# Kernel tuning notes

Hardware: AMD Instinct MI355X
Metric: run time of the kernel (lower is better)

## Reference

```python
import jax, jax.numpy as jnp
import numpy as np


def setup_inputs() -> dict:
    key = jax.random.key(0)
    ks = jax.random.split(key, 8)
    B, S, K, D = 2, 64, 64, 256
    C = D // 8
    return {
        "x": jax.random.normal(ks[0], (B, S, K, D), dtype=jnp.float32),
        "Wq": jax.random.normal(ks[1], (C, D), dtype=jnp.float32) * (1.0 / np.sqrt(D)),
        "bq": jax.random.normal(ks[2], (C,), dtype=jnp.float32) * 0.01,
        "Wk": jax.random.normal(ks[3], (C, D), dtype=jnp.float32) * (1.0 / np.sqrt(D)),
        "bk": jax.random.normal(ks[4], (C,), dtype=jnp.float32) * 0.01,
        "Wv": jax.random.normal(ks[5], (D, D), dtype=jnp.float32) * (1.0 / np.sqrt(D)),
        "bv": jax.random.normal(ks[6], (D,), dtype=jnp.float32) * 0.01,
        "gamma": jax.random.uniform(ks[7], (1,), dtype=jnp.float32),
    }


def reference(x, Wq, bq, Wk, bk, Wv, bv, gamma):
    # x: [B, S, K, D]
    B, S, K, D = x.shape
    N = K * S
    # torch: x.permute(0,3,2,1) -> [B, D, K, S]; flatten (K,S) -> N (n = k*S + s)
    xp = jnp.transpose(x, (0, 3, 2, 1)).reshape(B, D, N)  # [B, D, N]
    # 1x1 convs == per-token linear maps over the channel dim
    q = jnp.einsum('cd,bdn->bnc', Wq, xp) + bq            # [B, N, C]
    k = jnp.einsum('cd,bdn->bcn', Wk, xp) + bk[:, None]   # [B, C, N]
    energy = jnp.einsum('bnc,bcm->bnm', q, k)             # [B, N, N]
    attention = jax.nn.softmax(energy, axis=-1)           # rows sum to 1
    v = jnp.einsum('ed,bdn->ben', Wv, xp) + bv[:, None]   # [B, D, N]
    # out[b,d,i] = sum_j V[b,d,j] * A[b,i,j]
    out = jnp.einsum('bdj,bij->bdi', v, attention)        # [B, D, N]
    out = gamma * out + xp                                # residual with learned scale
    out = out.reshape(B, D, K, S)
    return jnp.transpose(out, (0, 3, 2, 1))               # [B, S, K, D]
```

## Files before the change

kernel.cpp:

```cpp
#include <hip/hip_runtime.h>
#include <stdint.h>
#include <math.h>

using short8   = __attribute__((ext_vector_type(8))) short;
using ushort4v = __attribute__((ext_vector_type(4))) unsigned short;
using f32x4    = __attribute__((ext_vector_type(4))) float;
using uint4v   = __attribute__((ext_vector_type(4))) unsigned int;
using uint2v   = __attribute__((ext_vector_type(2))) unsigned int;

#define B_ 2
#define S_ 64
#define K_ 64
#define D_ 256
#define C_ 32
#define N_ 4096
#define LOG2E 1.4426950408889634f

__device__ __forceinline__ float b2f(unsigned short u) {
    unsigned int v = ((unsigned int)u) << 16;
    return __builtin_bit_cast(float, v);
}
__device__ __forceinline__ unsigned short f2b(float f) {
    unsigned int x = __builtin_bit_cast(unsigned int, f);
    x += 0x7fffu + ((x >> 16) & 1u);
    return (unsigned short)(x >> 16);
}
__device__ __forceinline__ unsigned int pk2(float a, float b) {
    unsigned int xa = __builtin_bit_cast(unsigned int, a);
    unsigned int xb = __builtin_bit_cast(unsigned int, b);
    xa += 0x7fffu + ((xa >> 16) & 1u);
    xb += 0x7fffu + ((xb >> 16) & 1u);
    return (xa >> 16) | (xb & 0xffff0000u);
}

__global__ __launch_bounds__(256) void wcvt_kernel(
    const float* __restrict__ Wq, const float* __restrict__ bq,
    const float* __restrict__ Wk, const float* __restrict__ bk,
    const float* __restrict__ Wv, const float* __restrict__ bv,
    unsigned short* __restrict__ Wh, unsigned short* __restrict__ Wl,
    float* __restrict__ bcat)
{
    int oc = blockIdx.x;
    int d  = threadIdx.x;
    float w;
    if (oc < 32)       w = Wq[oc * 256 + d] * LOG2E;
    else if (oc < 64)  w = Wk[(oc - 32) * 256 + d];
    else               w = Wv[(oc - 64) * 256 + d];
    unsigned short h = f2b(w);
    Wh[oc * 256 + d] = h;
    Wl[oc * 256 + d] = f2b(w - b2f(h));
    if (d == 0) {
        float bb;
        if (oc < 32)      bb = bq[oc] * LOG2E;
        else if (oc < 64) bb = bk[oc - 32];
        else              bb = bv[oc - 64];
        bcat[oc] = bb;
    }
}

__global__ __launch_bounds__(512) void qkv_kernel(
    const float* __restrict__ x,
    const unsigned short* __restrict__ Wh, const unsigned short* __restrict__ Wl,
    const float* __restrict__ bcat,
    unsigned short* __restrict__ Qh, unsigned short* __restrict__ Ql,
    unsigned short* __restrict__ Kh, unsigned short* __restrict__ Kl,
    unsigned short* __restrict__ Vm)
{
    __shared__ unsigned short lxh[16 * 256];
    __shared__ unsigned short lxl[16 * 256];

    int tid = threadIdx.x;
    int bid = blockIdx.x;
    int b  = bid >> 8;
    int n0 = (bid & 255) << 4;

    {
        int tt = tid >> 5, m = tid & 31;
        int n = n0 + tt;
        int s = n & 63, kk = n >> 6;
        const float* xr = x + (((size_t)(b * S_ + s)) * K_ + kk) * D_ + m * 8;
        short8 h8, l8;
#pragma unroll
        for (int e = 0; e < 8; ++e) {
            float v = xr[e];
            unsigned short hh = f2b(v);
            h8[e] = (short)hh; l8[e] = (short)f2b(v - b2f(hh));
        }
        int sw = ((m ^ (tt & 7)) << 3);
        *(short8*)(lxh + tt * 256 + sw) = h8;
        *(short8*)(lxl + tt * 256 + sw) = l8;
    }
    __syncthreads();

    int wave = tid >> 6, lane = tid & 63;
    int col = lane & 15, g = lane >> 4;

    if (wave < 4) {
        int ct = wave;
        int oc0 = ct * 16;
        const unsigned short* whr = Wh + (size_t)(oc0 + col) * 256;
        const unsigned short* wlr = Wl + (size_t)(oc0 + col) * 256;
        f32x4 acc = {0.f, 0.f, 0.f, 0.f};
#pragma unroll
        for (int dc = 0; dc < 8; ++dc) {
            int sw = (((dc * 4 + g) ^ (col & 7)) << 3);
            short8 xh8 = *(const short8*)(lxh + col * 256 + sw);
            short8 xl8 = *(const short8*)(lxl + col * 256 + sw);
            short8 wh8 = *(const short8*)(whr + dc * 32 + g * 8);
            short8 wl8 = *(const short8*)(wlr + dc * 32 + g * 8);
            acc = __builtin_amdgcn_mfma_f32_16x16x32_bf16(xl8, wh8, acc, 0, 0, 0);
            acc = __builtin_amdgcn_mfma_f32_16x16x32_bf16(xh8, wl8, acc, 0, 0, 0);
            acc = __builtin_amdgcn_mfma_f32_16x16x32_bf16(xh8, wh8, acc, 0, 0, 0);
        }
        float bb = bcat[oc0 + col];
        unsigned short* Th = (ct < 2) ? Qh : Kh;
        unsigned short* Tl = (ct < 2) ? Ql : Kl;
        int c0 = (ct & 1) * 16;
#pragma unroll
        for (int r = 0; r < 4; ++r) {
            int tok = n0 + g * 4 + r;
            float v = acc[r] + bb;
            unsigned short hh = f2b(v);
            size_t idx = ((size_t)b * N_ + tok) * C_ + c0 + col;
            Th[idx] = hh;
            Tl[idx] = f2b(v - b2f(hh));
        }
    } else {
        int i = wave - 4;
#pragma unroll
        for (int k = 0; k < 4; ++k) {
            int ct = 4 + i + 4 * k;
            int oc0 = ct * 16;
            const unsigned short* whr = Wh + (size_t)(oc0 + col) * 256;
            f32x4 acc = {0.f, 0.f, 0.f, 0.f};
#pragma unroll
            for (int dc = 0; dc < 8; ++dc) {
                int sw = (((dc * 4 + g) ^ (col & 7)) << 3);
                short8 xh8 = *(const short8*)(lxh + col * 256 + sw);
                short8 wh8 = *(const short8*)(whr + dc * 32 + g * 8);
                acc = __builtin_amdgcn_mfma_f32_16x16x32_bf16(xh8, wh8, acc, 0, 0, 0);
            }
            float bb = bcat[oc0 + col];
            int c0 = oc0 - 64;
            ushort4v st;
#pragma unroll
            for (int r = 0; r < 4; ++r) st[r] = f2b(acc[r] + bb);
            int tok0 = n0 + g * 4;
            int s0 = 8 * g + ((n0 & 16) >> 2);
            int d_ch = c0 + col;
            int o = d_ch * 64 + s0 * 2;
            o ^= (d_ch & 7) << 4;
            size_t vbyteoff = ((size_t)b * (N_ / 32) + (tok0 >> 5)) * (D_ * 32 * 2)
                            + (size_t)o;
            *(ushort4v*)((char*)Vm + vbyteoff) = st;
        }
    }
}

__global__ __launch_bounds__(1024, 4) void attn_kernel(
    const unsigned short* __restrict__ Qh, const unsigned short* __restrict__ Ql,
    const unsigned short* __restrict__ Kh, const unsigned short* __restrict__ Kl,
    const unsigned short* __restrict__ Vm,
    unsigned short* __restrict__ O_bf16, float* __restrict__ lsum_part)
{
    __shared__ __align__(16) char vlds[2][16384];
    __shared__ __align__(16) char plds[2 * 8192];

    int tid  = threadIdx.x;
    int wave = tid >> 6;
    int lane = tid & 63;
    int col = lane & 15, g = lane >> 4;
    int qq = wave >> 2;
    int dq = wave & 3;
    int kh = dq & 1;
    int qs_own = dq >> 1;
    int tid16 = tid * 16;
    int lane16 = lane * 16;

    int bid = blockIdx.x;
    int x7 = bid & 7;
    int b  = x7 >> 2;
    int ks = x7 & 3;
    int qt = bid >> 3;
    int q0 = qt * 128 + qq * 32;
    int jbase = ks * (N_ / 4);

    size_t qoff = ((size_t)b * N_ + q0 + qs_own * 16 + col) * C_ + g * 8;
    short8 qfh = *(const short8*)(Qh + qoff);
    short8 qfl = *(const short8*)(Ql + qoff);

    f32x4 acc[2][4];
#pragma unroll
    for (int qs = 0; qs < 2; ++qs)
#pragma unroll
        for (int dt = 0; dt < 4; ++dt) acc[qs][dt] = (f32x4){0.f, 0.f, 0.f, 0.f};
    float l_run = 0.f;

    const unsigned short* kbh = Kh + (size_t)b * N_ * C_;
    const unsigned short* kbl = Kl + (size_t)b * N_ * C_;
    const char* vbyte = (const char*)Vm + (size_t)b * ((size_t)N_ * D_ * 2);

    auto kaddr = [&](int it) {
        return (size_t)(jbase + it * 32 + kh * 16 + col) * C_ + g * 8;
    };

    unsigned vro = (unsigned)(((dq * 64 + col) * 64 + g * 16) ^ ((col & 7) << 4));
    int st = qq * 2 + qs_own;
    char* pmy = plds + st * 1024 + lane16 + kh * 8;
    const char* pr0 = plds + (qq * 2) * 1024 + lane16;
    const char* pr1 = plds + (qq * 2 + 1) * 1024 + lane16;

    {
        const char* vsrc = vbyte + (size_t)(ks * 32) * 16384 + tid16;
        *(f32x4*)(vlds[0] + tid16) = *(const f32x4*)(vsrc);
    }
    short8 khA = *(const short8*)(kbh + kaddr(0));
    short8 klA = *(const short8*)(kbl + kaddr(0));
    short8 khB = *(const short8*)(kbh + kaddr(1));
    short8 klB = *(const short8*)(kbl + kaddr(1));
    {
        f32x4 z = {0.f, 0.f, 0.f, 0.f};
        f32x4 sa = __builtin_amdgcn_mfma_f32_16x16x32_bf16(klA, qfh, z, 0, 0, 0);
        sa = __builtin_amdgcn_mfma_f32_16x16x32_bf16(khA, qfl, sa, 0, 0, 0);
        sa = __builtin_amdgcn_mfma_f32_16x16x32_bf16(khA, qfh, sa, 0, 0, 0);
        float pa[4];
#pragma unroll
        for (int r = 0; r < 4; ++r) pa[r] = exp2f(sa[r]);
        l_run += (pa[0] + pa[1]) + (pa[2] + pa[3]);
        uint2v uo;
        uo[0] = pk2(pa[0], pa[1]); uo[1] = pk2(pa[2], pa[3]);
        *(uint2v*)(pmy) = uo;
    }
    __syncthreads();

#define ATTN_PHASE(IT, CKH, CKL, NKH, NKL)                                       \
    {                                                                            \
        int itn_ = (IT) + 1;                                                     \
        int itk_ = (IT) + 2;         \
        const char* vsrc_ = vbyte + (size_t)(ks * 32 + itn_) * 16384 + tid16;    \
        f32x4 stg_ = *(const f32x4*)(vsrc_);                                     \
        NKH = *(const short8*)(kbh + kaddr(itk_));                               \
        NKL = *(const short8*)(kbl + kaddr(itk_));                               \
        __builtin_amdgcn_sched_barrier(0);        \
        f32x4 z_ = {0.f, 0.f, 0.f, 0.f};                                         \
        __builtin_amdgcn_s_setprio(1);                                           \
        f32x4 sa_ = __builtin_amdgcn_mfma_f32_16x16x32_bf16(CKL, qfh, z_, 0, 0, 0); \
        sa_ = __builtin_amdgcn_mfma_f32_16x16x32_bf16(CKH, qfl, sa_, 0, 0, 0);   \
        sa_ = __builtin_amdgcn_mfma_f32_16x16x32_bf16(CKH, qfh, sa_, 0, 0, 0);   \
        __builtin_amdgcn_s_setprio(0);                                           \
        float pa_[4];                                                            \
        _Pragma("unroll")                                                        \
        for (int r = 0; r < 4; ++r) pa_[r] = exp2f(sa_[r]);                      \
        l_run += (pa_[0] + pa_[1]) + (pa_[2] + pa_[3]);                          \
        uint2v uo_;                                                              \
        uo_[0] = pk2(pa_[0], pa_[1]); uo_[1] = pk2(pa_[2], pa_[3]);              \
        int rb_ = (IT) & 1, wb_ = (itn_) & 1;                                    \
        short8 pf0_ = *(const short8*)(pr0 + rb_ * 8192);                        \
        short8 pf1_ = *(const short8*)(pr1 + rb_ * 8192);                        \
        short8 vf_[4];                                                           \
        _Pragma("unroll")                                                        \
        for (int dt = 0; dt < 4; ++dt)                                           \
            vf_[dt] = *(const short8*)(vlds[rb_] + vro + dt * 1024);             \
        __builtin_amdgcn_s_setprio(1);                                           \
        _Pragma("unroll")                                                        \
        for (int dt = 0; dt < 4; ++dt) {                                         \
            acc[0][dt] = __builtin_amdgcn_mfma_f32_16x16x32_bf16(vf_[dt], pf0_, acc[0][dt], 0, 0, 0); \
            acc[1][dt] = __builtin_amdgcn_mfma_f32_16x16x32_bf16(vf_[dt], pf1_, acc[1][dt], 0, 0, 0); \
        }                                                                        \
        __builtin_amdgcn_s_setprio(0);                                           \
        *(uint2v*)(pmy + wb_ * 8192) = uo_;                                      \
        *(f32x4*)(vlds[wb_] + tid16) = stg_;                                     \
        __syncthreads();                                                         \
    }

    for (int it2 = 0; it2 < 15; ++it2) {
        int itA = it2 * 2, itB = itA + 1;
        ATTN_PHASE(itA, khB, klB, khA, klA);
        ATTN_PHASE(itB, khA, klA, khB, klB);
    }
    ATTN_PHASE(30, khB, klB, khA, klA);
#undef ATTN_PHASE

    {
        short8 pf0 = *(const short8*)(pr0 + 8192);
        short8 pf1 = *(const short8*)(pr1 + 8192);
        short8 vf[4];
#pragma unroll
        for (int dt = 0; dt < 4; ++dt)
            vf[dt] = *(const short8*)(vlds[1] + vro + dt * 1024);
#pragma unroll
        for (int dt = 0; dt < 4; ++dt) {
            acc[0][dt] = __builtin_amdgcn_mfma_f32_16x16x32_bf16(vf[dt], pf0, acc[0][dt], 0, 0, 0);
            acc[1][dt] = __builtin_amdgcn_mfma_f32_16x16x32_bf16(vf[dt], pf1, acc[1][dt], 0, 0, 0);
        }
    }

    l_run += __shfl_xor(l_run, 16); l_run += __shfl_xor(l_run, 32);

    unsigned short* op = O_bf16 + (size_t)bid * 32768 + (qq * 2 + (dq >> 1)) * 4096;
#pragma unroll
    for (int qs = 0; qs < 2; ++qs)
#pragma unroll
        for (int dt = 0; dt < 4; ++dt) {
            int j = qs * 8 + (dq & 1) * 4 + dt;
            uint2v uo;
            uo[0] = pk2(acc[qs][dt][0], acc[qs][dt][1]);
            uo[1] = pk2(acc[qs][dt][2], acc[qs][dt][3]);
            *(uint2v*)(op + j * 256 + col * 16 + g * 4) = uo;
        }
    if (g == 0)
        lsum_part[bid * 256 + kh * 128 + qq * 32 + qs_own * 16 + col] = l_run;
}

__global__ __launch_bounds__(256) void epi_kernel(
    const unsigned short* __restrict__ O_bf16, const float* __restrict__ lsum_part,
    const float* __restrict__ x, const float* __restrict__ gamma_p,
    float* __restrict__ out)
{
    int gid = blockIdx.x * 256 + threadIdx.x;
    int d  = (gid & 63) * 4;
    int nl = gid >> 6;
    int b  = nl >> 12;
    int n  = nl & (N_ - 1);

    int qt = n >> 7, qq = (n >> 5) & 3, qs = (n >> 4) & 1, col = n & 15;
    int dh = d >> 7, dt = (d >> 4) & 7;
    int w = qq * 2 + dh, j = qs * 8 + dt;
    int boff = w * 4096 + j * 256 + col * 16 + (d & 15);
    int loff = qq * 32 + qs * 16 + col;

    f32x4 acc = {0.f, 0.f, 0.f, 0.f};
    float l = 0.f;
#pragma unroll
    for (int ks = 0; ks < 4; ++ks) {
        int bid = qt * 8 + b * 4 + ks;
        ushort4v p = *(const ushort4v*)(O_bf16 + (size_t)bid * 32768 + boff);
        acc[0] += b2f(p[0]); acc[1] += b2f(p[1]);
        acc[2] += b2f(p[2]); acc[3] += b2f(p[3]);
        l += lsum_part[bid * 256 + loff] + lsum_part[bid * 256 + 128 + loff];
    }
    float scale = gamma_p[0] / l;
    int s = n & 63, kk = n >> 6;
    size_t o = (((size_t)(b * S_ + s)) * K_ + kk) * D_ + d;
    f32x4 xv = *(const f32x4*)(x + o);
    f32x4 ov;
#pragma unroll
    for (int e = 0; e < 4; ++e) ov[e] = acc[e] * scale + xv[e];
    *(f32x4*)(out + o) = ov;
}

extern "C" void kernel_launch(void* const* d_in, const int* in_sizes, int n_in,
                              void* d_out, int out_size, void* d_ws, size_t ws_size,
                              hipStream_t stream) {
    const float* x  = (const float*)d_in[0];
    const float* Wq = (const float*)d_in[1];
    const float* bq = (const float*)d_in[2];
    const float* Wk = (const float*)d_in[3];
    const float* bk = (const float*)d_in[4];
    const float* Wv = (const float*)d_in[5];
    const float* bv = (const float*)d_in[6];
    const float* gm = (const float*)d_in[7];

    char* ws = (char*)d_ws;
    unsigned short* Wh   = (unsigned short*)(ws);
    unsigned short* Wl   = (unsigned short*)(ws + 0x40000);
    float*          bcat = (float*)         (ws + 0x80000);
    unsigned short* Qh   = (unsigned short*)(ws + 0x100000);
    unsigned short* Ql   = (unsigned short*)(ws + 0x180000);
    unsigned short* Kh   = (unsigned short*)(ws + 0x200000);
    unsigned short* Kl   = (unsigned short*)(ws + 0x280000);
    unsigned short* Vm   = (unsigned short*)(ws + 0x300000);
    unsigned short* Op   = (unsigned short*)(ws + 0x700000);
    float*          lp   = (float*)         (ws + 0x2700000);
    float* o = (float*)d_out;

    wcvt_kernel<<<320, 256, 0, stream>>>(Wq, bq, Wk, bk, Wv, bv, Wh, Wl, bcat);
    qkv_kernel<<<512, 512, 0, stream>>>(x, Wh, Wl, bcat, Qh, Ql, Kh, Kl, Vm);
    attn_kernel<<<256, 1024, 0, stream>>>(Qh, Ql, Kh, Kl, Vm, Op, lp);
    epi_kernel<<<2048, 256, 0, stream>>>(Op, lp, x, gm, o);
}
```

Measured before the change: 62.83 us.

## Halve attention block to 512 threads with each wave owning more work

The attention kernel now runs 8 waves per block instead of 16. Each wave computes scores for both 16-key halves of its query strip and accumulates PV for four query strips instead of two. This removes the duplicated key-half split and cuts barrier participants and redundant V-fragment LDS reads per block. In exchange each wave holds twice the accumulators and does more sequential MFMA work, with fewer waves left to hide latency. The lsum partial layout and the epilogue indexing change to match.

```diff
diff --git a/kernel.cpp b/kernel.cpp
--- a/kernel.cpp
+++ b/kernel.cpp
@@ -157,7 +157,7 @@
     }
 }
 
-__global__ __launch_bounds__(1024, 4) void attn_kernel(
+__global__ __launch_bounds__(512, 2) void attn_kernel(
     const unsigned short* __restrict__ Qh, const unsigned short* __restrict__ Ql,
     const unsigned short* __restrict__ Kh, const unsigned short* __restrict__ Kl,
     const unsigned short* __restrict__ Vm,
@@ -170,11 +170,10 @@
     int wave = tid >> 6;
     int lane = tid & 63;
     int col = lane & 15, g = lane >> 4;
-    int qq = wave >> 2;
-    int dq = wave & 3;
-    int kh = dq & 1;
-    int qs_own = dq >> 1;
-    int tid16 = tid * 16;
+    int qq2 = wave >> 2;
+    int dq  = wave & 3;
+    int st_own = qq2 * 4 + dq;
+    int tid32 = tid * 32;
     int lane16 = lane * 16;
 
     int bid = blockIdx.x;
@@ -182,134 +181,154 @@
     int b  = x7 >> 2;
     int ks = x7 & 3;
     int qt = bid >> 3;
-    int q0 = qt * 128 + qq * 32;
     int jbase = ks * (N_ / 4);
 
-    size_t qoff = ((size_t)b * N_ + q0 + qs_own * 16 + col) * C_ + g * 8;
+    size_t qoff = ((size_t)b * N_ + qt * 128 + st_own * 16 + col) * C_ + g * 8;
     short8 qfh = *(const short8*)(Qh + qoff);
     short8 qfl = *(const short8*)(Ql + qoff);
 
-    f32x4 acc[2][4];
-#pragma unroll
-    for (int qs = 0; qs < 2; ++qs)
-#pragma unroll
-        for (int dt = 0; dt < 4; ++dt) acc[qs][dt] = (f32x4){0.f, 0.f, 0.f, 0.f};
+    f32x4 acc[4][4];
+#pragma unroll
+    for (int s = 0; s < 4; ++s)
+#pragma unroll
+        for (int dt = 0; dt < 4; ++dt) acc[s][dt] = (f32x4){0.f, 0.f, 0.f, 0.f};
     float l_run = 0.f;
 
     const unsigned short* kbh = Kh + (size_t)b * N_ * C_;
     const unsigned short* kbl = Kl + (size_t)b * N_ * C_;
     const char* vbyte = (const char*)Vm + (size_t)b * ((size_t)N_ * D_ * 2);
 
-    auto kaddr = [&](int it) {
-        return (size_t)(jbase + it * 32 + kh * 16 + col) * C_ + g * 8;
+    auto kaddr = [&](int it, int half) {
+        return (size_t)(jbase + it * 32 + half * 16 + col) * C_ + g * 8;
     };
 
     unsigned vro = (unsigned)(((dq * 64 + col) * 64 + g * 16) ^ ((col & 7) << 4));
-    int st = qq * 2 + qs_own;
-    char* pmy = plds + st * 1024 + lane16 + kh * 8;
-    const char* pr0 = plds + (qq * 2) * 1024 + lane16;
-    const char* pr1 = plds + (qq * 2 + 1) * 1024 + lane16;
+    char* pmy = plds + st_own * 1024 + lane16;
+    const char* prg = plds + (qq2 * 4) * 1024 + lane16;
 
     {
-        const char* vsrc = vbyte + (size_t)(ks * 32) * 16384 + tid16;
-        *(f32x4*)(vlds[0] + tid16) = *(const f32x4*)(vsrc);
-    }
-    short8 khA = *(const short8*)(kbh + kaddr(0));
-    short8 klA = *(const short8*)(kbl + kaddr(0));
-    short8 khB = *(const short8*)(kbh + kaddr(1));
-    short8 klB = *(const short8*)(kbl + kaddr(1));
+        const char* vsrc = vbyte + (size_t)(ks * 32) * 16384 + tid32;
+        *(f32x4*)(vlds[0] + tid32)      = *(const f32x4*)(vsrc);
+        *(f32x4*)(vlds[0] + tid32 + 16) = *(const f32x4*)(vsrc + 16);
+    }
+    short8 k0hA = *(const short8*)(kbh + kaddr(0, 0));
+    short8 k0lA = *(const short8*)(kbl + kaddr(0, 0));
+    short8 k1hA = *(const short8*)(kbh + kaddr(0, 1));
+    short8 k1lA = *(const short8*)(kbl + kaddr(0, 1));
+    short8 k0hB = *(const short8*)(kbh + kaddr(1, 0));
+    short8 k0lB = *(const short8*)(kbl + kaddr(1, 0));
+    short8 k1hB = *(const short8*)(kbh + kaddr(1, 1));
+    short8 k1lB = *(const short8*)(kbl + kaddr(1, 1));
     {
         f32x4 z = {0.f, 0.f, 0.f, 0.f};
-        f32x4 sa = __builtin_amdgcn_mfma_f32_16x16x32_bf16(klA, qfh, z, 0, 0, 0);
-        sa = __builtin_amdgcn_mfma_f32_16x16x32_bf16(khA, qfl, sa, 0, 0, 0);
-        sa = __builtin_amdgcn_mfma_f32_16x16x32_bf16(khA, qfh, sa, 0, 0, 0);
-        float pa[4];
-#pragma unroll
-        for (int r = 0; r < 4; ++r) pa[r] = exp2f(sa[r]);
-        l_run += (pa[0] + pa[1]) + (pa[2] + pa[3]);
-        uint2v uo;
-        uo[0] = pk2(pa[0], pa[1]); uo[1] = pk2(pa[2], pa[3]);
-        *(uint2v*)(pmy) = uo;
+        f32x4 s0 = __builtin_amdgcn_mfma_f32_16x16x32_bf16(k0lA, qfh, z, 0, 0, 0);
+        s0 = __builtin_amdgcn_mfma_f32_16x16x32_bf16(k0hA, qfl, s0, 0, 0, 0);
+        s0 = __builtin_amdgcn_mfma_f32_16x16x32_bf16(k0hA, qfh, s0, 0, 0, 0);
+        f32x4 s1 = __builtin_amdgcn_mfma_f32_16x16x32_bf16(k1lA, qfh, z, 0, 0, 0);
+        s1 = __builtin_amdgcn_mfma_f32_16x16x32_bf16(k1hA, qfl, s1, 0, 0, 0);
+        s1 = __builtin_amdgcn_mfma_f32_16x16x32_bf16(k1hA, qfh, s1, 0, 0, 0);
+        float p0[4], p1[4];
+#pragma unroll
+        for (int r = 0; r < 4; ++r) { p0[r] = exp2f(s0[r]); p1[r] = exp2f(s1[r]); }
+        l_run += (p0[0] + p0[1]) + (p0[2] + p0[3]) + (p1[0] + p1[1]) + (p1[2] + p1[3]);
+        uint4v uo;
+        uo[0] = pk2(p0[0], p0[1]); uo[1] = pk2(p0[2], p0[3]);
+        uo[2] = pk2(p1[0], p1[1]); uo[3] = pk2(p1[2], p1[3]);
+        *(uint4v*)(pmy) = uo;
     }
     __syncthreads();
 
-#define ATTN_PHASE(IT, CKH, CKL, NKH, NKL)                                       \
+#define ATTN_PHASE(IT, C0H, C0L, C1H, C1L, N0H, N0L, N1H, N1L)                   \
     {                                                                            \
         int itn_ = (IT) + 1;                                                     \
         int itk_ = (IT) + 2;         \
-        const char* vsrc_ = vbyte + (size_t)(ks * 32 + itn_) * 16384 + tid16;    \
-        f32x4 stg_ = *(const f32x4*)(vsrc_);                                     \
-        NKH = *(const short8*)(kbh + kaddr(itk_));                               \
-        NKL = *(const short8*)(kbl + kaddr(itk_));                               \
+        const char* vsrc_ = vbyte + (size_t)(ks * 32 + itn_) * 16384 + tid32;    \
+        f32x4 stg0_ = *(const f32x4*)(vsrc_);                                    \
+        f32x4 stg1_ = *(const f32x4*)(vsrc_ + 16);                               \
+        N0H = *(const short8*)(kbh + kaddr(itk_, 0));                            \
+        N0L = *(const short8*)(kbl + kaddr(itk_, 0));                            \
+        N1H = *(const short8*)(kbh + kaddr(itk_, 1));                            \
+        N1L = *(const short8*)(kbl + kaddr(itk_, 1));                            \
         __builtin_amdgcn_sched_barrier(0);        \
         f32x4 z_ = {0.f, 0.f, 0.f, 0.f};                                         \
         __builtin_amdgcn_s_setprio(1);                                           \
-        f32x4 sa_ = __builtin_amdgcn_mfma_f32_16x16x32_bf16(CKL, qfh, z_, 0, 0, 0); \
-        sa_ = __builtin_amdgcn_mfma_f32_16x16x32_bf16(CKH, qfl, sa_, 0, 0, 0);   \
-        sa_ = __builtin_amdgcn_mfma_f32_16x16x32_bf16(CKH, qfh, sa_, 0, 0, 0);   \
+        f32x4 s0_ = __builtin_amdgcn_mfma_f32_16x16x32_bf16(C0L, qfh, z_, 0, 0, 0); \
+        s0_ = __builtin_amdgcn_mfma_f32_16x16x32_bf16(C0H, qfl, s0_, 0, 0, 0);   \
+        s0_ = __builtin_amdgcn_mfma_f32_16x16x32_bf16(C0H, qfh, s0_, 0, 0, 0);   \
+        f32x4 s1_ = __builtin_amdgcn_mfma_f32_16x16x32_bf16(C1L, qfh, z_, 0, 0, 0); \
+        s1_ = __builtin_amdgcn_mfma_f32_16x16x32_bf16(C1H, qfl, s1_, 0, 0, 0);   \
+        s1_ = __builtin_amdgcn_mfma_f32_16x16x32_bf16(C1H, qfh, s1_, 0, 0, 0);   \
         __builtin_amdgcn_s_setprio(0);                                           \
-        float pa_[4];                                                            \
+        float p0_[4], p1_[4];                                                    \
         _Pragma("unroll")                                                        \
-        for (int r = 0; r < 4; ++r) pa_[r] = exp2f(sa_[r]);                      \
-        l_run += (pa_[0] + pa_[1]) + (pa_[2] + pa_[3]);                          \
-        uint2v uo_;                                                              \
-        uo_[0] = pk2(pa_[0], pa_[1]); uo_[1] = pk2(pa_[2], pa_[3]);              \
+        for (int r = 0; r < 4; ++r) { p0_[r] = exp2f(s0_[r]); p1_[r] = exp2f(s1_[r]); } \
+        l_run += (p0_[0] + p0_[1]) + (p0_[2] + p0_[3])                           \
+               + (p1_[0] + p1_[1]) + (p1_[2] + p1_[3]);                          \
+        uint4v uo_;                                                              \
+        uo_[0] = pk2(p0_[0], p0_[1]); uo_[1] = pk2(p0_[2], p0_[3]);              \
+        uo_[2] = pk2(p1_[0], p1_[1]); uo_[3] = pk2(p1_[2], p1_[3]);              \
         int rb_ = (IT) & 1, wb_ = (itn_) & 1;                                    \
-        short8 pf0_ = *(const short8*)(pr0 + rb_ * 8192);                        \
-        short8 pf1_ = *(const short8*)(pr1 + rb_ * 8192);                        \
-        short8 vf_[4];                                                           \
+        short8 pf_[4], vf_[4];                                                   \
+        _Pragma("unroll")                                                        \
+        for (int s = 0; s < 4; ++s)                                              \
+            pf_[s] = *(const short8*)(prg + s * 1024 + rb_ * 8192);              \
         _Pragma("unroll")                                                        \
         for (int dt = 0; dt < 4; ++dt)                                           \
             vf_[dt] = *(const short8*)(vlds[rb_] + vro + dt * 1024);             \
         __builtin_amdgcn_s_setprio(1);                                           \
         _Pragma("unroll")                                                        \
-        for (int dt = 0; dt < 4; ++dt) {                                         \
-            acc[0][dt] = __builtin_amdgcn_mfma_f32_16x16x32_bf16(vf_[dt], pf0_, acc[0][dt], 0, 0, 0); \
-            acc[1][dt] = __builtin_amdgcn_mfma_f32_16x16x32_bf16(vf_[dt], pf1_, acc[1][dt], 0, 0, 0); \
-        }                                                                        \
+        for (int s = 0; s < 4; ++s)                                              \
+            _Pragma("unroll")                                                    \
+            for (int dt = 0; dt < 4; ++dt)                                       \
+                acc[s][dt] = __builtin_amdgcn_mfma_f32_16x16x32_bf16(vf_[dt], pf_[s], acc[s][dt], 0, 0, 0); \
         __builtin_amdgcn_s_setprio(0);                                           \
-        *(uint2v*)(pmy + wb_ * 8192) = uo_;                                      \
-        *(f32x4*)(vlds[wb_] + tid16) = stg_;                                     \
+        *(uint4v*)(pmy + wb_ * 8192) = uo_;                                      \
+        *(f32x4*)(vlds[wb_] + tid32)      = stg0_;                               \
+        *(f32x4*)(vlds[wb_] + tid32 + 16) = stg1_;                               \
         __syncthreads();                                                         \
     }
 
     for (int it2 = 0; it2 < 15; ++it2) {
         int itA = it2 * 2, itB = itA + 1;
-        ATTN_PHASE(itA, khB, klB, khA, klA);
-        ATTN_PHASE(itB, khA, klA, khB, klB);
-    }
-    ATTN_PHASE(30, khB, klB, khA, klA);
+        ATTN_PHASE(itA, k0hB, k0lB, k1hB, k1lB, k0hA, k0lA, k1hA, k1lA);
+        ATTN_PHASE(itB, k0hA, k0lA, k1hA, k1lA, k0hB, k0lB, k1hB, k1lB);
+    }
+    ATTN_PHASE(30, k0hB, k0lB, k1hB, k1lB, k0hA, k0lA, k1hA, k1lA);
 #undef ATTN_PHASE
 
     {
-        short8 pf0 = *(const short8*)(pr0 + 8192);
-        short8 pf1 = *(const short8*)(pr1 + 8192);
-        short8 vf[4];
+        short8 pf[4], vf[4];
+#pragma unroll
+        for (int s = 0; s < 4; ++s)
+            pf[s] = *(const short8*)(prg + s * 1024 + 8192);
 #pragma unroll
         for (int dt = 0; dt < 4; ++dt)
             vf[dt] = *(const short8*)(vlds[1] + vro + dt * 1024);
 #pragma unroll
+        for (int s = 0; s < 4; ++s)
+#pragma unroll
+            for (int dt = 0; dt < 4; ++dt)
+                acc[s][dt] = __builtin_amdgcn_mfma_f32_16x16x32_bf16(vf[dt], pf[s], acc[s][dt], 0, 0, 0);
+    }
+
+    l_run += __shfl_xor(l_run, 16); l_run += __shfl_xor(l_run, 32);
+
+    unsigned short* ob = O_bf16 + (size_t)bid * 32768;
+#pragma unroll
+    for (int s = 0; s < 4; ++s) {
+        int stg = qq2 * 4 + s;
+        unsigned short* op = ob + ((stg >> 1) * 2 + (dq >> 1)) * 4096;
+#pragma unroll
         for (int dt = 0; dt < 4; ++dt) {
-            acc[0][dt] = __builtin_amdgcn_mfma_f32_16x16x32_bf16(vf[dt], pf0, acc[0][dt], 0, 0, 0);
-            acc[1][dt] = __builtin_amdgcn_mfma_f32_16x16x32_bf16(vf[dt], pf1, acc[1][dt], 0, 0, 0);
-        }
-    }
-
-    l_run += __shfl_xor(l_run, 16); l_run += __shfl_xor(l_run, 32);
-
-    unsigned short* op = O_bf16 + (size_t)bid * 32768 + (qq * 2 + (dq >> 1)) * 4096;
-#pragma unroll
-    for (int qs = 0; qs < 2; ++qs)
-#pragma unroll
-        for (int dt = 0; dt < 4; ++dt) {
-            int j = qs * 8 + (dq & 1) * 4 + dt;
+            int j = (stg & 1) * 8 + (dq & 1) * 4 + dt;
             uint2v uo;
-            uo[0] = pk2(acc[qs][dt][0], acc[qs][dt][1]);
-            uo[1] = pk2(acc[qs][dt][2], acc[qs][dt][3]);
+            uo[0] = pk2(acc[s][dt][0], acc[s][dt][1]);
+            uo[1] = pk2(acc[s][dt][2], acc[s][dt][3]);
             *(uint2v*)(op + j * 256 + col * 16 + g * 4) = uo;
         }
+    }
     if (g == 0)
-        lsum_part[bid * 256 + kh * 128 + qq * 32 + qs_own * 16 + col] = l_run;
+        lsum_part[bid * 128 + st_own * 16 + col] = l_run;
 }
 
 __global__ __launch_bounds__(256) void epi_kernel(
@@ -327,7 +346,7 @@
     int dh = d >> 7, dt = (d >> 4) & 7;
     int w = qq * 2 + dh, j = qs * 8 + dt;
     int boff = w * 4096 + j * 256 + col * 16 + (d & 15);
-    int loff = qq * 32 + qs * 16 + col;
+    int loff = ((n >> 4) & 7) * 16 + col;
 
     f32x4 acc = {0.f, 0.f, 0.f, 0.f};
     float l = 0.f;
@@ -337,7 +356,7 @@
         ushort4v p = *(const ushort4v*)(O_bf16 + (size_t)bid * 32768 + boff);
         acc[0] += b2f(p[0]); acc[1] += b2f(p[1]);
         acc[2] += b2f(p[2]); acc[3] += b2f(p[3]);
-        l += lsum_part[bid * 256 + loff] + lsum_part[bid * 256 + 128 + loff];
+        l += lsum_part[bid * 128 + loff];
     }
     float scale = gamma_p[0] / l;
     int s = n & 63, kk = n >> 6;
@@ -376,6 +395,6 @@
 
     wcvt_kernel<<<320, 256, 0, stream>>>(Wq, bq, Wk, bk, Wv, bv, Wh, Wl, bcat);
     qkv_kernel<<<512, 512, 0, stream>>>(x, Wh, Wl, bcat, Qh, Ql, Kh, Kl, Vm);
-    attn_kernel<<<256, 1024, 0, stream>>>(Qh, Ql, Kh, Kl, Vm, Op, lp);
+    attn_kernel<<<256, 512, 0, stream>>>(Qh, Ql, Kh, Kl, Vm, Op, lp);
     epi_kernel<<<2048, 256, 0, stream>>>(Op, lp, x, gm, o);
 }
```

Measured after the change: 65.24 us. 1.04x slower.
